# Optimization experiments

Measured on AMD Instinct MI355X. Metric: run time of the kernel, lower is better.

Reference implementation:

```python
import jax, jax.numpy as jnp
import numpy as np

N = 50000
E = 800000
F_IN = 64
F_OUT = 64


def setup_inputs() -> dict:
    key = jax.random.key(0)
    ks = jax.random.split(key, 14)
    x = jax.random.normal(ks[0], (N, F_IN), dtype=jnp.float32)
    row_low = jax.random.randint(ks[1], (E,), 0, N)
    col_low = jax.random.randint(ks[2], (E,), 0, N)
    val_low = jax.random.uniform(ks[3], (E,), dtype=jnp.float32)
    row_high = jax.random.randint(ks[4], (E,), 0, N)
    col_high = jax.random.randint(ks[5], (E,), 0, N)
    val_high = jax.random.uniform(ks[6], (E,), dtype=jnp.float32)
    # xavier-uniform style init for weights
    def xavier(k, shape):
        fan_in, fan_out = shape[0], shape[1]
        bound = float(np.sqrt(6.0 / (fan_in + fan_out)))
        return jax.random.uniform(k, shape, jnp.float32, -bound, bound)
    W_low = xavier(ks[7], (F_IN, F_OUT))
    W_high = xavier(ks[8], (F_IN, F_OUT))
    W_mlp = xavier(ks[9], (F_IN, F_OUT))
    a_low = xavier(ks[10], (F_OUT, 1))
    a_high = xavier(ks[11], (F_OUT, 1))
    a_mlp = xavier(ks[12], (F_OUT, 1))
    att3 = xavier(ks[13], (3, 3))
    return dict(x=x, row_low=row_low, col_low=col_low, val_low=val_low,
                row_high=row_high, col_high=col_high, val_high=val_high,
                W_low=W_low, W_high=W_high, W_mlp=W_mlp,
                a_low=a_low, a_high=a_high, a_mlp=a_mlp, att3=att3)


def _spmm(row, col, val, h, n):
    # (sparse adj) @ h : gather source rows, scale by edge weight, scatter-add to dest
    return jax.ops.segment_sum(val[:, None] * h[col], row, num_segments=n)


def reference(x, row_low, col_low, val_low, row_high, col_high, val_high,
              W_low, W_high, W_mlp, a_low, a_high, a_mlp, att3):
    n = x.shape[0]
    out_low = jax.nn.relu(_spmm(row_low, col_low, val_low, x @ W_low, n))
    out_high = jax.nn.relu(_spmm(row_high, col_high, val_high, x @ W_high, n))
    out_mlp = jax.nn.relu(x @ W_mlp)
    T = 3.0
    feats = jnp.concatenate([out_low @ a_low, out_high @ a_high, out_mlp @ a_mlp], axis=1)  # [N,3]
    logits = (jax.nn.sigmoid(feats) @ att3) / T
    att = jax.nn.softmax(logits, axis=1)  # [N,3]
    return 3.0 * (att[:, 0:1] * out_low + att[:, 1:2] * out_high + att[:, 2:3] * out_mlp)
```

## Files before the change

### kernel.cpp

```cpp
#include <hip/hip_runtime.h>
#include <hip/hip_fp16.h>


#define NNODE 50000
#define NEDGE 800000
#define NBUCK 782
#define CAP   1552

typedef __attribute__((ext_vector_type(8))) short short8v;
typedef __attribute__((ext_vector_type(4))) float float4v;

__device__ __forceinline__ unsigned short f2bf(float f) {
    unsigned u = __float_as_uint(f);
    u += 0x7FFFu + ((u >> 16) & 1u);
    return (unsigned short)(u >> 16);
}
__device__ __forceinline__ __half2 u_as_h2(unsigned u) {
    return *reinterpret_cast<__half2*>(&u);
}

__global__ __launch_bounds__(256)
void zero_kernel(unsigned int* __restrict__ g)
{
    const int i = blockIdx.x * 256 + threadIdx.x;
    if (i < 2 * NBUCK) g[i] = 0u;
}

__global__ __launch_bounds__(256)
void gemm_mfma_kernel(const float* __restrict__ x,
                      const float* __restrict__ Wl, const float* __restrict__ Wh,
                      const float* __restrict__ Wm,
                      unsigned short* __restrict__ hl16,
                      unsigned short* __restrict__ hh16,
                      unsigned short* __restrict__ hm16)
{
    __shared__ unsigned short wt[3][64][72];
    const int t = threadIdx.x;
#pragma unroll 1
    for (int m = 0; m < 3; ++m) {
        const float* __restrict__ W = (m == 0) ? Wl : (m == 1) ? Wh : Wm;
        for (int i = t; i < 4096; i += 256) {
            const int k = i >> 6, c = i & 63;
            wt[m][c][k] = f2bf(W[i]);
        }
    }
    __syncthreads();

    const int wid = t >> 6, lane = t & 63;
    const int node0 = blockIdx.x * 64 + wid * 16;
    if (node0 >= NNODE) return;
    const int arow = lane & 15;
    const int hi = lane >> 4;

    const float* __restrict__ xr = x + (size_t)(node0 + arow) * 64 + hi * 8;
    const float4 pa0 = *(const float4*)(xr + 0);
    const float4 pa1 = *(const float4*)(xr + 4);
    const float4 pb0 = *(const float4*)(xr + 32);
    const float4 pb1 = *(const float4*)(xr + 36);
    short8v a0, a1;
    a0[0] = (short)f2bf(pa0.x); a0[1] = (short)f2bf(pa0.y);
    a0[2] = (short)f2bf(pa0.z); a0[3] = (short)f2bf(pa0.w);
    a0[4] = (short)f2bf(pa1.x); a0[5] = (short)f2bf(pa1.y);
    a0[6] = (short)f2bf(pa1.z); a0[7] = (short)f2bf(pa1.w);
    a1[0] = (short)f2bf(pb0.x); a1[1] = (short)f2bf(pb0.y);
    a1[2] = (short)f2bf(pb0.z); a1[3] = (short)f2bf(pb0.w);
    a1[4] = (short)f2bf(pb1.x); a1[5] = (short)f2bf(pb1.y);
    a1[6] = (short)f2bf(pb1.z); a1[7] = (short)f2bf(pb1.w);

#pragma unroll 1
    for (int m = 0; m < 3; ++m) {
        unsigned short* __restrict__ H = (m == 0) ? hl16 : (m == 1) ? hh16 : hm16;
        float4v acc0 = {0.f, 0.f, 0.f, 0.f}, acc1 = {0.f, 0.f, 0.f, 0.f};
        float4v acc2 = {0.f, 0.f, 0.f, 0.f}, acc3 = {0.f, 0.f, 0.f, 0.f};

#define DO_CT(CT, ACC)                                                          \
        {                                                                       \
            const short8v b0 = *(const short8v*)&wt[m][CT * 16 + arow][hi * 8]; \
            const short8v b1 = *(const short8v*)&wt[m][CT * 16 + arow][32 + hi * 8]; \
            ACC = __builtin_amdgcn_mfma_f32_16x16x32_bf16(a0, b0, ACC, 0, 0, 0); \
            ACC = __builtin_amdgcn_mfma_f32_16x16x32_bf16(a1, b1, ACC, 0, 0, 0); \
        }
        DO_CT(0, acc0) DO_CT(1, acc1) DO_CT(2, acc2) DO_CT(3, acc3)
#undef DO_CT

        const bool rl = (m == 2);
#define ST_CT(CT, ACC)                                                          \
        {                                                                       \
            _Pragma("unroll")                                                   \
            for (int r = 0; r < 4; ++r) {                                       \
                float v = ACC[r];                                               \
                if (rl) v = fmaxf(v, 0.f);                                      \
                H[(size_t)(node0 + hi * 4 + r) * 64 + CT * 16 + arow] =         \
                    __half_as_ushort(__float2half(v));                          \
            }                                                                   \
        }
        ST_CT(0, acc0) ST_CT(1, acc1) ST_CT(2, acc2) ST_CT(3, acc3)
#undef ST_CT
    }
}

__global__ __launch_bounds__(512)
void scatter_kernel(const int* __restrict__ row_low, const int* __restrict__ col_low,
                    const float* __restrict__ val_low,
                    const int* __restrict__ row_high, const int* __restrict__ col_high,
                    const float* __restrict__ val_high,
                    unsigned int* __restrict__ gcursor,
                    unsigned int* __restrict__ rec4,
                    unsigned char* __restrict__ row8)
{
    __shared__ unsigned int hist_s[2 * NBUCK];
    __shared__ unsigned int base_s[2 * NBUCK];
    const int t = threadIdx.x;
    const int ebase = blockIdx.x * 8192;

    for (int i = t; i < 2 * NBUCK; i += 512) hist_s[i] = 0u;
    __syncthreads();

    int rows[16]; unsigned int rank[16];
#pragma unroll
    for (int j = 0; j < 16; ++j) {
        const int e = ebase + j * 512 + t;
        rows[j] = 0; rank[j] = 0u;
        if (e < 2 * NEDGE) {
            const int r = (e < NEDGE) ? row_low[e] : row_high[e - NEDGE];
            const int fb = ((e < NEDGE) ? 0 : NBUCK) + (r >> 6);
            rows[j] = r;
            rank[j] = atomicAdd(&hist_s[fb], 1u);
        }
    }
    __syncthreads();
    for (int i = t; i < 2 * NBUCK; i += 512) {
        const unsigned int c = hist_s[i];
        base_s[i] = c ? atomicAdd(&gcursor[i], c) : 0u;
    }
    __syncthreads();
#pragma unroll
    for (int j = 0; j < 16; ++j) {
        const int e = ebase + j * 512 + t;
        if (e < 2 * NEDGE) {
            const int g = (e >= NEDGE);
            const int ee = e - g * NEDGE;
            const int r = rows[j];
            const int c = g ? col_high[ee] : col_low[ee];
            const float v = g ? val_high[ee] : val_low[ee];
            const int fb = g * NBUCK + (r >> 6);
            const unsigned int pos = base_s[fb] + rank[j];
            if (pos < CAP) {
                const unsigned short hb = __half_as_ushort(__float2half(v));
                const size_t slot = (size_t)fb * CAP + pos;
                rec4[slot] = (unsigned)c | ((unsigned)hb << 16);
                row8[slot] = (unsigned char)(r & 63);
            }
        }
    }
}

__global__ __launch_bounds__(256)
void sort_kernel(unsigned int* __restrict__ rec4,
                 const unsigned char* __restrict__ row8,
                 const unsigned int* __restrict__ gcursor,
                 int* __restrict__ rs, int* __restrict__ rc)
{
    __shared__ unsigned int rec_s[CAP];
    __shared__ unsigned char row_s[CAP];
    __shared__ unsigned int hist[64];
    __shared__ unsigned int offs[64];
    __shared__ unsigned int cur[64];

    const int fb = blockIdx.x;
    const int t = threadIdx.x;
    unsigned int* __restrict__ seg = rec4 + (size_t)fb * CAP;
    const unsigned char* __restrict__ rseg = row8 + (size_t)fb * CAP;
    int cnt = (int)gcursor[fb];
    if (cnt > CAP) cnt = CAP;

    if (t < 64) { hist[t] = 0u; cur[t] = 0u; }
    __syncthreads();

    for (int i = t; i < cnt; i += 256) {
        rec_s[i] = seg[i];
        const unsigned char r = rseg[i];
        row_s[i] = r;
        atomicAdd(&hist[r], 1u);
    }
    __syncthreads();

    if (t < 64) {
        const int pv = (int)((hist[t] + 7u) & ~7u);
        int xsc = pv;
#pragma unroll
        for (int d = 1; d < 64; d <<= 1) {
            int y = __shfl_up(xsc, d, 64);
            if (t >= d) xsc += y;
        }
        offs[t] = (unsigned)(xsc - pv);
    }
    __syncthreads();

    for (int i = t; i < cnt; i += 256) {
        const unsigned r = row_s[i];
        const unsigned pos = offs[r] + atomicAdd(&cur[r], 1u);
        if (pos < CAP) seg[pos] = rec_s[i];
    }
    if (t < 64) {
        const unsigned b = offs[t] + hist[t];
        const unsigned e = offs[t] + ((hist[t] + 7u) & ~7u);
        for (unsigned u = b; u < e && u < CAP; ++u) seg[u] = 0u;
    }

    if (t < 64) {
        const int g = (fb >= NBUCK);
        const int node = ((fb - g * NBUCK) << 6) + t;
        if (node < NNODE) {
            const unsigned P = (hist[t] + 7u) & ~7u;
            const int avail = CAP - (int)offs[t];
            int nq = (int)(P >> 2);
            int nqa = avail > 0 ? ((avail >> 2) & ~1) : 0;
            if (nq > nqa) nq = nqa;
            rs[g * NNODE + node] = fb * CAP + (int)offs[t];
            rc[g * NNODE + node] = nq;
        }
    }
}

__global__ __launch_bounds__(256, 8)
void spmm_finalize_kernel(const unsigned int* __restrict__ rec4,
                          const int* __restrict__ rs, const int* __restrict__ rc,
                          const unsigned short* __restrict__ hl16,
                          const unsigned short* __restrict__ hh16,
                          const unsigned short* __restrict__ hm16,
                          const float* __restrict__ aL, const float* __restrict__ aH,
                          const float* __restrict__ aM, const float* __restrict__ att3,
                          float* __restrict__ out)
{
    const int wid = threadIdx.x >> 6;
    const int lane = threadIdx.x & 63;
    const int sub = lane >> 4;
    const int f4 = (lane & 15) << 2;
    const unsigned fb2 = (unsigned)(f4 * 2);
    const int node = blockIdx.x * 4 + wid;
    if (node >= NNODE) return;

    const int sL = __builtin_amdgcn_readfirstlane(rs[node]);
    const int nqL = __builtin_amdgcn_readfirstlane(rc[node]);
    const int sH = __builtin_amdgcn_readfirstlane(rs[NNODE + node]);
    const int nqH = __builtin_amdgcn_readfirstlane(rc[NNODE + node]);
    const unsigned int* __restrict__ segL = rec4 + sL + sub;
    const unsigned int* __restrict__ segH = rec4 + sH + sub;
    const int nqm = (nqL > nqH) ? nqL : nqH;

    const __half2 hz2 = u_as_h2(0u);
    __half2 aL0a = hz2, aL1a = hz2, aL0b = hz2, aL1b = hz2;
    __half2 aH0a = hz2, aH1a = hz2, aH0b = hz2, aH1b = hz2;

#pragma unroll 1
    for (int q = 0; q < nqm; q += 2) {
        const unsigned rL0 = segL[q * 4];
        const unsigned rL1 = segL[q * 4 + 4];
        const unsigned rH0 = segH[q * 4];
        const unsigned rH1 = segH[q * 4 + 4];
        const uint2 uL0 = *(const uint2*)((const char*)hl16 + (size_t)(((rL0 & 0xFFFFu) << 7) + fb2));
        const uint2 uL1 = *(const uint2*)((const char*)hl16 + (size_t)(((rL1 & 0xFFFFu) << 7) + fb2));
        const uint2 uH0 = *(const uint2*)((const char*)hh16 + (size_t)(((rH0 & 0xFFFFu) << 7) + fb2));
        const uint2 uH1 = *(const uint2*)((const char*)hh16 + (size_t)(((rH1 & 0xFFFFu) << 7) + fb2));
        __builtin_amdgcn_sched_barrier(0);
        const unsigned dL0 = (rL0 & 0xFFFF0000u) | (rL0 >> 16);
        const unsigned dL1 = (rL1 & 0xFFFF0000u) | (rL1 >> 16);
        const unsigned dH0 = (rH0 & 0xFFFF0000u) | (rH0 >> 16);
        const unsigned dH1 = (rH1 & 0xFFFF0000u) | (rH1 >> 16);
        const __half2 vL0 = u_as_h2((q     < nqL) ? dL0 : 0u);
        const __half2 vL1 = u_as_h2((q + 1 < nqL) ? dL1 : 0u);
        const __half2 vH0 = u_as_h2((q     < nqH) ? dH0 : 0u);
        const __half2 vH1 = u_as_h2((q + 1 < nqH) ? dH1 : 0u);
        aL0a = __hfma2(u_as_h2(uL0.x), vL0, aL0a);
        aL1a = __hfma2(u_as_h2(uL0.y), vL0, aL1a);
        aL0b = __hfma2(u_as_h2(uL1.x), vL1, aL0b);
        aL1b = __hfma2(u_as_h2(uL1.y), vL1, aL1b);
        aH0a = __hfma2(u_as_h2(uH0.x), vH0, aH0a);
        aH1a = __hfma2(u_as_h2(uH0.y), vH0, aH1a);
        aH0b = __hfma2(u_as_h2(uH1.x), vH1, aH0b);
        aH1b = __hfma2(u_as_h2(uH1.y), vH1, aH1b);
    }

    float lx = __low2float(aL0a) + __low2float(aL0b);
    float ly = __high2float(aL0a) + __high2float(aL0b);
    float lz = __low2float(aL1a) + __low2float(aL1b);
    float lw = __high2float(aL1a) + __high2float(aL1b);
    float hx = __low2float(aH0a) + __low2float(aH0b);
    float hy = __high2float(aH0a) + __high2float(aH0b);
    float hz = __low2float(aH1a) + __low2float(aH1b);
    float hw = __high2float(aH1a) + __high2float(aH1b);

    lx += __shfl_xor(lx, 16, 64); ly += __shfl_xor(ly, 16, 64);
    lz += __shfl_xor(lz, 16, 64); lw += __shfl_xor(lw, 16, 64);
    hx += __shfl_xor(hx, 16, 64); hy += __shfl_xor(hy, 16, 64);
    hz += __shfl_xor(hz, 16, 64); hw += __shfl_xor(hw, 16, 64);
    lx += __shfl_xor(lx, 32, 64); ly += __shfl_xor(ly, 32, 64);
    lz += __shfl_xor(lz, 32, 64); lw += __shfl_xor(lw, 32, 64);
    hx += __shfl_xor(hx, 32, 64); hy += __shfl_xor(hy, 32, 64);
    hz += __shfl_xor(hz, 32, 64); hw += __shfl_xor(hw, 32, 64);

    const float olx = fmaxf(lx, 0.f), oly = fmaxf(ly, 0.f);
    const float olz = fmaxf(lz, 0.f), olw = fmaxf(lw, 0.f);
    const float ohx = fmaxf(hx, 0.f), ohy = fmaxf(hy, 0.f);
    const float ohz = fmaxf(hz, 0.f), ohw = fmaxf(hw, 0.f);

    const uint2 om2 = *(const uint2*)&hm16[(size_t)node * 64 + f4];
    const float omx = __low2float(u_as_h2(om2.x));
    const float omy = __high2float(u_as_h2(om2.x));
    const float omz = __low2float(u_as_h2(om2.y));
    const float omw = __high2float(u_as_h2(om2.y));

    const float4 aL4 = *(const float4*)&aL[f4];
    const float4 aH4 = *(const float4*)&aH[f4];
    const float4 aM4 = *(const float4*)&aM[f4];

    float f0 = olx * aL4.x + oly * aL4.y + olz * aL4.z + olw * aL4.w;
    float f1 = ohx * aH4.x + ohy * aH4.y + ohz * aH4.z + ohw * aH4.w;
    float f2 = omx * aM4.x + omy * aM4.y + omz * aM4.z + omw * aM4.w;
#pragma unroll
    for (int msk = 1; msk < 16; msk <<= 1) {
        f0 += __shfl_xor(f0, msk, 64);
        f1 += __shfl_xor(f1, msk, 64);
        f2 += __shfl_xor(f2, msk, 64);
    }
    const float s0 = 1.f / (1.f + __expf(-f0));
    const float s1 = 1.f / (1.f + __expf(-f1));
    const float s2 = 1.f / (1.f + __expf(-f2));
    const float invT = 1.f / 3.f;
    const float l0g = (s0 * att3[0] + s1 * att3[3] + s2 * att3[6]) * invT;
    const float l1g = (s0 * att3[1] + s1 * att3[4] + s2 * att3[7]) * invT;
    const float l2g = (s0 * att3[2] + s1 * att3[5] + s2 * att3[8]) * invT;
    const float mx = fmaxf(l0g, fmaxf(l1g, l2g));
    const float e0 = __expf(l0g - mx);
    const float e1 = __expf(l1g - mx);
    const float e2 = __expf(l2g - mx);
    const float inv = 1.f / (e0 + e1 + e2);
    const float wl = 3.f * inv * e0, wh = 3.f * inv * e1, wm = 3.f * inv * e2;

    if (lane < 16) {
        float4 o;
        o.x = wl * olx + wh * ohx + wm * omx;
        o.y = wl * oly + wh * ohy + wm * omy;
        o.z = wl * olz + wh * ohz + wm * omz;
        o.w = wl * olw + wh * ohw + wm * omw;
        *(float4*)&out[(size_t)node * 64 + f4] = o;
    }
}

extern "C" void kernel_launch(void* const* d_in, const int* in_sizes, int n_in,
                              void* d_out, int out_size, void* d_ws, size_t ws_size,
                              hipStream_t stream)
{
    const float* x        = (const float*)d_in[0];
    const int*   row_low  = (const int*)  d_in[1];
    const int*   col_low  = (const int*)  d_in[2];
    const float* val_low  = (const float*)d_in[3];
    const int*   row_high = (const int*)  d_in[4];
    const int*   col_high = (const int*)  d_in[5];
    const float* val_high = (const float*)d_in[6];
    const float* W_low    = (const float*)d_in[7];
    const float* W_high   = (const float*)d_in[8];
    const float* W_mlp    = (const float*)d_in[9];
    const float* a_low    = (const float*)d_in[10];
    const float* a_high   = (const float*)d_in[11];
    const float* a_mlp    = (const float*)d_in[12];
    const float* att3     = (const float*)d_in[13];
    float* out = (float*)d_out;

    const size_t NM = (size_t)NNODE * 64;
    const size_t NSLOT = (size_t)2 * NBUCK * CAP;

    unsigned short* hl16    = (unsigned short*)d_ws;
    unsigned short* hh16    = hl16 + NM;
    unsigned short* hm16    = hh16 + NM;
    unsigned int*   rec4    = (unsigned int*)(hm16 + NM);
    unsigned char*  row8    = (unsigned char*)(rec4 + NSLOT);
    unsigned int*   gcursor = (unsigned int*)(row8 + ((NSLOT + 3) & ~size_t(3)));
    int*            rs      = (int*)(gcursor + 2 * NBUCK);
    int*            rc      = rs + 2 * NNODE;

    zero_kernel<<<(2 * NBUCK + 255) / 256, 256, 0, stream>>>(gcursor);

    scatter_kernel<<<(2 * NEDGE + 8191) / 8192, 512, 0, stream>>>(
        row_low, col_low, val_low, row_high, col_high, val_high,
        gcursor, rec4, row8);

    gemm_mfma_kernel<<<(NNODE + 63) / 64, 256, 0, stream>>>(
        x, W_low, W_high, W_mlp, hl16, hh16, hm16);

    sort_kernel<<<2 * NBUCK, 256, 0, stream>>>(rec4, row8, gcursor, rs, rc);

    spmm_finalize_kernel<<<(NNODE + 3) / 4, 256, 0, stream>>>(
        rec4, rs, rc, hl16, hh16, hm16, a_low, a_high, a_mlp, att3, out);
}
```

Baseline: 95.69 us.

## Widen row buckets to 128 nodes and pack edge records into one 8-byte store

Halves the number of row buckets (128 nodes each instead of 64) and raises per-bucket capacity to match. The scatter pass now writes one uint2 per edge (column, local row, half-precision value) into a separate staging buffer instead of two arrays. The sort pass reads that buffer and writes the sorted records to a distinct output array. The sort scan is extended to 128 rows using a two-wavefront prefix with a shared partial sum. This aims to cut global atomic contention and the number of small scattered writes, at the cost of more workspace, fewer sort blocks and larger shared-memory segments.

```diff
diff --git a/kernel.cpp b/kernel.cpp
--- a/kernel.cpp
+++ b/kernel.cpp
@@ -4,8 +4,8 @@
 
 #define NNODE 50000
 #define NEDGE 800000
-#define NBUCK 782
-#define CAP   1552
+#define NBUCK 391
+#define CAP   2880
 
 typedef __attribute__((ext_vector_type(8))) short short8v;
 typedef __attribute__((ext_vector_type(4))) float float4v;
@@ -104,9 +104,7 @@
                     const float* __restrict__ val_low,
                     const int* __restrict__ row_high, const int* __restrict__ col_high,
                     const float* __restrict__ val_high,
-                    unsigned int* __restrict__ gcursor,
-                    unsigned int* __restrict__ rec4,
-                    unsigned char* __restrict__ row8)
+                    unsigned int* __restrict__ gcursor, uint2* __restrict__ packed)
 {
     __shared__ unsigned int hist_s[2 * NBUCK];
     __shared__ unsigned int base_s[2 * NBUCK];
@@ -123,7 +121,7 @@
         rows[j] = 0; rank[j] = 0u;
         if (e < 2 * NEDGE) {
             const int r = (e < NEDGE) ? row_low[e] : row_high[e - NEDGE];
-            const int fb = ((e < NEDGE) ? 0 : NBUCK) + (r >> 6);
+            const int fb = ((e < NEDGE) ? 0 : NBUCK) + (r >> 7);
             rows[j] = r;
             rank[j] = atomicAdd(&hist_s[fb], 1u);
         }
@@ -143,74 +141,82 @@
             const int r = rows[j];
             const int c = g ? col_high[ee] : col_low[ee];
             const float v = g ? val_high[ee] : val_low[ee];
-            const int fb = g * NBUCK + (r >> 6);
+            const int fb = g * NBUCK + (r >> 7);
             const unsigned int pos = base_s[fb] + rank[j];
             if (pos < CAP) {
-                const unsigned short hb = __half_as_ushort(__float2half(v));
-                const size_t slot = (size_t)fb * CAP + pos;
-                rec4[slot] = (unsigned)c | ((unsigned)hb << 16);
-                row8[slot] = (unsigned char)(r & 63);
+                uint2 pk;
+                pk.x = (unsigned int)c | ((unsigned int)(r & 127) << 16);
+                pk.y = (unsigned)__half_as_ushort(__float2half(v));
+                packed[(size_t)fb * CAP + pos] = pk;
             }
         }
     }
 }
 
 __global__ __launch_bounds__(256)
-void sort_kernel(unsigned int* __restrict__ rec4,
-                 const unsigned char* __restrict__ row8,
+void sort_kernel(const uint2* __restrict__ packed,
+                 unsigned int* __restrict__ rec4,
                  const unsigned int* __restrict__ gcursor,
                  int* __restrict__ rs, int* __restrict__ rc)
 {
     __shared__ unsigned int rec_s[CAP];
     __shared__ unsigned char row_s[CAP];
-    __shared__ unsigned int hist[64];
-    __shared__ unsigned int offs[64];
-    __shared__ unsigned int cur[64];
+    __shared__ unsigned int hist[128];
+    __shared__ unsigned int offs[128];
+    __shared__ unsigned int cur[128];
+    __shared__ unsigned int wsum2[2];
 
     const int fb = blockIdx.x;
     const int t = threadIdx.x;
-    unsigned int* __restrict__ seg = rec4 + (size_t)fb * CAP;
-    const unsigned char* __restrict__ rseg = row8 + (size_t)fb * CAP;
+    const uint2* __restrict__ seg = packed + (size_t)fb * CAP;
+    unsigned int* __restrict__ rout = rec4 + (size_t)fb * CAP;
     int cnt = (int)gcursor[fb];
     if (cnt > CAP) cnt = CAP;
 
-    if (t < 64) { hist[t] = 0u; cur[t] = 0u; }
+    if (t < 128) { hist[t] = 0u; cur[t] = 0u; }
     __syncthreads();
 
     for (int i = t; i < cnt; i += 256) {
-        rec_s[i] = seg[i];
-        const unsigned char r = rseg[i];
-        row_s[i] = r;
+        const uint2 p = seg[i];
+        const unsigned r = (p.x >> 16) & 127u;
+        rec_s[i] = (p.x & 0xFFFFu) | (p.y << 16);
+        row_s[i] = (unsigned char)r;
         atomicAdd(&hist[r], 1u);
     }
     __syncthreads();
 
-    if (t < 64) {
-        const int pv = (int)((hist[t] + 7u) & ~7u);
-        int xsc = pv;
+    unsigned pv = 0, xinc = 0;
+    if (t < 128) {
+        pv = (hist[t] + 7u) & ~7u;
+        xinc = pv;
 #pragma unroll
         for (int d = 1; d < 64; d <<= 1) {
-            int y = __shfl_up(xsc, d, 64);
-            if (t >= d) xsc += y;
-        }
-        offs[t] = (unsigned)(xsc - pv);
+            unsigned y = __shfl_up(xinc, d, 64);
+            if ((t & 63) >= d) xinc += y;
+        }
+        if ((t & 63) == 63) wsum2[t >> 6] = xinc;
+    }
+    __syncthreads();
+    if (t < 128) {
+        const unsigned add = (t >= 64) ? wsum2[0] : 0u;
+        offs[t] = add + xinc - pv;
     }
     __syncthreads();
 
     for (int i = t; i < cnt; i += 256) {
         const unsigned r = row_s[i];
         const unsigned pos = offs[r] + atomicAdd(&cur[r], 1u);
-        if (pos < CAP) seg[pos] = rec_s[i];
-    }
-    if (t < 64) {
+        if (pos < CAP) rout[pos] = rec_s[i];
+    }
+    if (t < 128) {
         const unsigned b = offs[t] + hist[t];
         const unsigned e = offs[t] + ((hist[t] + 7u) & ~7u);
-        for (unsigned u = b; u < e && u < CAP; ++u) seg[u] = 0u;
-    }
-
-    if (t < 64) {
+        for (unsigned u = b; u < e && u < CAP; ++u) rout[u] = 0u;
+    }
+
+    if (t < 128) {
         const int g = (fb >= NBUCK);
-        const int node = ((fb - g * NBUCK) << 6) + t;
+        const int node = ((fb - g * NBUCK) << 7) + t;
         if (node < NNODE) {
             const unsigned P = (hist[t] + 7u) & ~7u;
             const int avail = CAP - (int)offs[t];
@@ -374,22 +380,21 @@
     unsigned short* hl16    = (unsigned short*)d_ws;
     unsigned short* hh16    = hl16 + NM;
     unsigned short* hm16    = hh16 + NM;
-    unsigned int*   rec4    = (unsigned int*)(hm16 + NM);
-    unsigned char*  row8    = (unsigned char*)(rec4 + NSLOT);
-    unsigned int*   gcursor = (unsigned int*)(row8 + ((NSLOT + 3) & ~size_t(3)));
+    uint2*          packed  = (uint2*)(hm16 + NM);
+    unsigned int*   rec4    = (unsigned int*)(packed + NSLOT);
+    unsigned int*   gcursor = rec4 + NSLOT;
     int*            rs      = (int*)(gcursor + 2 * NBUCK);
     int*            rc      = rs + 2 * NNODE;
 
     zero_kernel<<<(2 * NBUCK + 255) / 256, 256, 0, stream>>>(gcursor);
 
     scatter_kernel<<<(2 * NEDGE + 8191) / 8192, 512, 0, stream>>>(
-        row_low, col_low, val_low, row_high, col_high, val_high,
-        gcursor, rec4, row8);
+        row_low, col_low, val_low, row_high, col_high, val_high, gcursor, packed);
 
     gemm_mfma_kernel<<<(NNODE + 63) / 64, 256, 0, stream>>>(
         x, W_low, W_high, W_mlp, hl16, hh16, hm16);
 
-    sort_kernel<<<2 * NBUCK, 256, 0, stream>>>(rec4, row8, gcursor, rs, rc);
+    sort_kernel<<<2 * NBUCK, 256, 0, stream>>>(packed, rec4, gcursor, rs, rc);
 
     spmm_finalize_kernel<<<(NNODE + 3) / 4, 256, 0, stream>>>(
         rec4, rs, rc, hl16, hh16, hm16, a_low, a_high, a_mlp, att3, out);
```

Result: faster. 90.62 us (-5.3%).
